# Kernel tuning notes

Hardware: AMD Instinct MI355X
Metric: run time of the kernel (lower is better)

## Reference

```python
import jax, jax.numpy as jnp
import numpy as np

EPS = 1.0 / 137.0  # fine-structure-constant epsilon used throughout the Yat ops


def yat_dense(x, W, b, alpha):
    # x: [..., C], W: [C, F] -> [..., F]
    dot = jnp.einsum('btc,cf->btf', x, W)
    x_norm = jnp.sum(x * x, axis=-1, keepdims=True)        # [..., 1]
    w_norm = jnp.sum(W * W, axis=0)                         # [F]
    dist = x_norm + w_norm - 2.0 * dot
    y = dot * dot / (dist + EPS)
    y = y + b
    F = W.shape[1]
    scale = (np.sqrt(F) / np.log(1.0 + F)) ** 1.0           # base; alpha exponent applied below
    return y * ((np.float32(np.sqrt(F)) / np.float32(np.log1p(F))) ** alpha)


def setup_inputs() -> dict:
    key = jax.random.key(0)
    ks = jax.random.split(key, 8)
    B, T, C = 4, 1024, 768
    x = jax.random.normal(ks[0], (B, T, C), dtype=jnp.float32)
    mask = jnp.tril(jnp.ones((T, T), dtype=bool))[None, None, :, :]  # causal [1,1,T,T]
    sd = 1.0 / np.sqrt(C)
    W_attn = jax.random.normal(ks[1], (C, 3 * C), dtype=jnp.float32) * sd
    b_attn = jnp.zeros((3 * C,), dtype=jnp.float32)
    alpha_attn = jnp.ones((), dtype=jnp.float32)
    W_proj = jax.random.normal(ks[2], (C, C), dtype=jnp.float32) * sd
    b_proj = jnp.zeros((C,), dtype=jnp.float32)
    alpha_proj = jnp.ones((), dtype=jnp.float32)
    return {"x": x, "mask": mask, "W_attn": W_attn, "b_attn": b_attn,
            "alpha_attn": alpha_attn, "W_proj": W_proj, "b_proj": b_proj,
            "alpha_proj": alpha_proj}


def reference(x, mask, W_attn, b_attn, alpha_attn, W_proj, b_proj, alpha_proj):
    B, T, C = x.shape
    H = 12
    D = C // H  # head_dim
    qkv = yat_dense(x, W_attn, b_attn, alpha_attn)          # [B,T,3C]
    qkv = qkv.reshape(B, T, 3 * H, D)
    q, k, v = jnp.array_split(qkv, 3, axis=2)
    q = jnp.transpose(q, (0, 2, 1, 3))                       # [B,H,T,D]
    k = jnp.transpose(k, (0, 2, 1, 3))
    v = jnp.transpose(v, (0, 2, 1, 3))
    scale = 1.0 / np.float32(np.sqrt(D))
    dot = jnp.einsum('bhid,bhjd->bhij', q, k)                # [B,H,T,T]
    sq_dot = jnp.square(dot * scale)
    q_norm = jnp.sum(jnp.square(q), axis=-1)[..., None]      # [B,H,T,1]
    k_norm = jnp.sum(jnp.square(k), axis=-1)[..., None, :]   # [B,H,1,T]
    sq_dist = q_norm + k_norm - 2.0 * dot * scale
    attn = sq_dot / (sq_dist + EPS)
    attn = jnp.where(mask, attn, jnp.finfo(jnp.float32).min)
    attn = jax.nn.softmax(attn, axis=-1)
    out = jnp.einsum('bhij,bhjd->bhid', attn, v)             # [B,H,T,D]
    out = jnp.transpose(out, (0, 2, 1, 3)).reshape(B, T, C)
    out = yat_dense(out, W_proj, b_proj, alpha_proj)         # [B,T,C]
    return out
```

## Files before the change

### kernel.cpp

```cpp
#include <hip/hip_runtime.h>
#include <math.h>

#define EPS_YAT (1.0f/137.0f)

typedef unsigned short u16;
typedef unsigned int u32;
typedef __attribute__((ext_vector_type(8))) __bf16 bf16x8;
typedef __attribute__((ext_vector_type(4))) float f32x4;

__device__ __forceinline__ float4 ld4(const float* p) { return *(const float4*)p; }

__device__ __forceinline__ u16 bf16_rne(float f) {
    u32 u = __float_as_uint(f);
    u32 r = (u + 0x7fffu + ((u >> 16) & 1u)) >> 16;
    return (u16)r;
}
__device__ __forceinline__ float bf16_f(u16 h) {
    return __uint_as_float(((u32)h) << 16);
}

__global__ void colnorm_part(const float* __restrict__ W, float* __restrict__ part,
                             int K, int N) {
    __shared__ float sm[256];
    const int col = blockIdx.x * 64 + (threadIdx.x & 63);
    const int q = threadIdx.x >> 6;
    const int rows = K >> 6;
    const int k0 = blockIdx.y * (K >> 4) + q * rows;
    float s = 0.f;
    for (int k = k0; k < k0 + rows; ++k) {
        float w = W[(size_t)k * N + col];
        s += w * w;
    }
    sm[threadIdx.x] = s;
    __syncthreads();
    if (threadIdx.x < 64)
        part[(size_t)blockIdx.y * N + col] =
            sm[threadIdx.x] + sm[threadIdx.x + 64] + sm[threadIdx.x + 128] + sm[threadIdx.x + 192];
}

__global__ void colnorm_reduce(const float* __restrict__ part, float* __restrict__ wn,
                               int N) {
    int gid = blockIdx.x * 256 + threadIdx.x;
    if (gid >= N) return;
    float s = 0.f;
    #pragma unroll
    for (int i = 0; i < 16; ++i) s += part[(size_t)i * N + gid];
    wn[gid] = s;
}

__global__ void rownorm_kernel(const float* __restrict__ X, float* __restrict__ rn, int K) {
    int wave = threadIdx.x >> 6;
    int lane = threadIdx.x & 63;
    int row = blockIdx.x * 4 + wave;
    const float* xr = X + (size_t)row * K;
    float s = 0.f;
    for (int k = lane * 4; k < K; k += 256) {
        float4 v = ld4(xr + k);
        s += v.x * v.x + v.y * v.y + v.z * v.z + v.w * v.w;
    }
    for (int off = 32; off; off >>= 1) s += __shfl_down(s, off);
    if (lane == 0) rn[row] = s;
}

__global__ void rownorm_hl(const u16* __restrict__ Xh, const u16* __restrict__ Xl,
                           float* __restrict__ rn) {
    int wave = threadIdx.x >> 6;
    int lane = threadIdx.x & 63;
    int row = blockIdx.x * 4 + wave;
    const u16* xh = Xh + (size_t)row * 768;
    const u16* xl = Xl + (size_t)row * 768;
    float s = 0.f;
    for (int k = lane * 4; k < 768; k += 256) {
        uint2 hv = *(const uint2*)(xh + k);
        uint2 lv = *(const uint2*)(xl + k);
        float a0 = bf16_f((u16)hv.x)         + bf16_f((u16)lv.x);
        float a1 = bf16_f((u16)(hv.x >> 16)) + bf16_f((u16)(lv.x >> 16));
        float a2 = bf16_f((u16)hv.y)         + bf16_f((u16)lv.y);
        float a3 = bf16_f((u16)(hv.y >> 16)) + bf16_f((u16)(lv.y >> 16));
        s += a0 * a0 + a1 * a1 + a2 * a2 + a3 * a3;
    }
    for (int off = 32; off; off >>= 1) s += __shfl_down(s, off);
    if (lane == 0) rn[row] = s;
}

__global__ void qknorm_kernel(const u16* __restrict__ qh, const u16* __restrict__ ql,
                              float* __restrict__ qn, float* __restrict__ kn) {
    int gid = blockIdx.x * 256 + threadIdx.x;
    int lane = gid & 15;
    int idx = gid >> 4;
    int which = (idx >= 49152) ? 1 : 0;
    int r = idx - which * 49152;
    int t = r & 1023;
    int bh = r >> 10;
    int h = bh % 12, b = bh / 12;
    const size_t off = (size_t)(b * 1024 + t) * 2304 + which * 768 + h * 64 + lane * 4;
    uint2 hv = *(const uint2*)(qh + off);
    uint2 lv = *(const uint2*)(ql + off);
    float a0 = bf16_f((u16)hv.x)         + bf16_f((u16)lv.x);
    float a1 = bf16_f((u16)(hv.x >> 16)) + bf16_f((u16)(lv.x >> 16));
    float a2 = bf16_f((u16)hv.y)         + bf16_f((u16)lv.y);
    float a3 = bf16_f((u16)(hv.y >> 16)) + bf16_f((u16)(lv.y >> 16));
    float s = a0 * a0 + a1 * a1 + a2 * a2 + a3 * a3;
    s += __shfl_xor(s, 1, 16);
    s += __shfl_xor(s, 2, 16);
    s += __shfl_xor(s, 4, 16);
    s += __shfl_xor(s, 8, 16);
    if (lane == 0) (which ? kn : qn)[r] = s;
}

__global__ void split_kernel(const float* __restrict__ X, u16* __restrict__ Xh,
                             u16* __restrict__ Xl, int n4) {
    int gid = blockIdx.x * 256 + threadIdx.x;
    if (gid >= n4) return;
    float4 v = ld4(X + (size_t)gid * 4);
    u16 h0 = bf16_rne(v.x), h1 = bf16_rne(v.y), h2 = bf16_rne(v.z), h3 = bf16_rne(v.w);
    u16 l0 = bf16_rne(v.x - bf16_f(h0));
    u16 l1 = bf16_rne(v.y - bf16_f(h1));
    u16 l2 = bf16_rne(v.z - bf16_f(h2));
    u16 l3 = bf16_rne(v.w - bf16_f(h3));
    uint2 hp, lp;
    hp.x = (u32)h0 | ((u32)h1 << 16); hp.y = (u32)h2 | ((u32)h3 << 16);
    lp.x = (u32)l0 | ((u32)l1 << 16); lp.y = (u32)l2 | ((u32)l3 << 16);
    *(uint2*)(Xh + (size_t)gid * 4) = hp;
    *(uint2*)(Xl + (size_t)gid * 4) = lp;
}

__global__ void split_wt_kernel(const float* __restrict__ W, u16* __restrict__ Th,
                                u16* __restrict__ Tl, int K, int N) {
    __shared__ float tile[64 * 68];
    const int tid = threadIdx.x;
    const int n0 = blockIdx.x << 6;
    const int k0 = blockIdx.y << 6;
    const int rr = tid >> 4;
    const int cc = (tid & 15) << 2;
    #pragma unroll
    for (int s = 0; s < 4; ++s) {
        int k_l = rr + s * 16;
        *(float4*)&tile[k_l * 68 + cc] = ld4(W + (size_t)(k0 + k_l) * N + n0 + cc);
    }
    __syncthreads();
    #pragma unroll
    for (int s = 0; s < 4; ++s) {
        int n_l = rr + s * 16;
        float a0 = tile[(cc + 0) * 68 + n_l];
        float a1 = tile[(cc + 1) * 68 + n_l];
        float a2 = tile[(cc + 2) * 68 + n_l];
        float a3 = tile[(cc + 3) * 68 + n_l];
        u16 h0 = bf16_rne(a0), h1 = bf16_rne(a1), h2 = bf16_rne(a2), h3 = bf16_rne(a3);
        u16 l0 = bf16_rne(a0 - bf16_f(h0));
        u16 l1 = bf16_rne(a1 - bf16_f(h1));
        u16 l2 = bf16_rne(a2 - bf16_f(h2));
        u16 l3 = bf16_rne(a3 - bf16_f(h3));
        uint2 hp, lp;
        hp.x = (u32)h0 | ((u32)h1 << 16); hp.y = (u32)h2 | ((u32)h3 << 16);
        lp.x = (u32)l0 | ((u32)l1 << 16); lp.y = (u32)l2 | ((u32)l3 << 16);
        size_t o = (size_t)(n0 + n_l) * K + k0 + cc;
        *(uint2*)(Th + o) = hp;
        *(uint2*)(Tl + o) = lp;
    }
}

template<int SPLIT>
__global__ __launch_bounds__(256, 2)
void yat_gemm_mfma(const u16* __restrict__ Ah, const u16* __restrict__ Al,
                   const u16* __restrict__ Bh, const u16* __restrict__ Bl,
                   const float* __restrict__ bias, const float* __restrict__ xn,
                   const float* __restrict__ wnc, const float* __restrict__ alphap,
                   const float Fdim, float* __restrict__ out,
                   u16* __restrict__ outh, u16* __restrict__ outl,
                   const int N, const int K) {
    __shared__ __align__(16) u16 lAh[128 * 40], lAl[128 * 40];
    __shared__ __align__(16) u16 lBh[128 * 40], lBl[128 * 40];
    const int tid = threadIdx.x;
    const int m0 = blockIdx.y << 7;
    const int n0 = blockIdx.x << 7;
    const int wave = tid >> 6;
    const int lane = tid & 63;
    const int wm = (wave >> 1) << 6;
    const int wnn = (wave & 1) << 6;
    const int lm = lane & 15;
    const int kq = lane >> 4;
    const int sr = tid >> 1;
    const int sh = (tid & 1) << 4;

    const u16* gAh = Ah + (size_t)(m0 + sr) * K + sh;
    const u16* gAl = Al + (size_t)(m0 + sr) * K + sh;
    const u16* gBh = Bh + (size_t)(n0 + sr) * K + sh;
    const u16* gBl = Bl + (size_t)(n0 + sr) * K + sh;

    f32x4 acc[4][4] = {};

    uint4 pA0 = *(const uint4*)(gAh), pA1 = *(const uint4*)(gAh + 8);
    uint4 pB0 = *(const uint4*)(gAl), pB1 = *(const uint4*)(gAl + 8);
    uint4 pC0 = *(const uint4*)(gBh), pC1 = *(const uint4*)(gBh + 8);
    uint4 pD0 = *(const uint4*)(gBl), pD1 = *(const uint4*)(gBl + 8);

    const int lw = sr * 40 + sh;
    for (int k0 = 0; k0 < K; k0 += 32) {
        __syncthreads();
        *(uint4*)&lAh[lw] = pA0; *(uint4*)&lAh[lw + 8] = pA1;
        *(uint4*)&lAl[lw] = pB0; *(uint4*)&lAl[lw + 8] = pB1;
        *(uint4*)&lBh[lw] = pC0; *(uint4*)&lBh[lw + 8] = pC1;
        *(uint4*)&lBl[lw] = pD0; *(uint4*)&lBl[lw + 8] = pD1;
        __syncthreads();
        if (k0 + 32 < K) {
            pA0 = *(const uint4*)(gAh + k0 + 32); pA1 = *(const uint4*)(gAh + k0 + 40);
            pB0 = *(const uint4*)(gAl + k0 + 32); pB1 = *(const uint4*)(gAl + k0 + 40);
            pC0 = *(const uint4*)(gBh + k0 + 32); pC1 = *(const uint4*)(gBh + k0 + 40);
            pD0 = *(const uint4*)(gBl + k0 + 32); pD1 = *(const uint4*)(gBl + k0 + 40);
        }

        bf16x8 fah[4], fal[4], fbh[4], fbl[4];
        #pragma unroll
        for (int i = 0; i < 4; ++i) {
            const int ra = (wm + i * 16 + lm) * 40 + kq * 8;
            fah[i] = *(const bf16x8*)&lAh[ra];
            fal[i] = *(const bf16x8*)&lAl[ra];
            const int rb = (wnn + i * 16 + lm) * 40 + kq * 8;
            fbh[i] = *(const bf16x8*)&lBh[rb];
            fbl[i] = *(const bf16x8*)&lBl[rb];
        }
        #pragma unroll
        for (int i = 0; i < 4; ++i)
            #pragma unroll
            for (int j = 0; j < 4; ++j) {
                f32x4 c = acc[i][j];
                c = __builtin_amdgcn_mfma_f32_16x16x32_bf16(fah[i], fbh[j], c, 0, 0, 0);
                c = __builtin_amdgcn_mfma_f32_16x16x32_bf16(fah[i], fbl[j], c, 0, 0, 0);
                c = __builtin_amdgcn_mfma_f32_16x16x32_bf16(fal[i], fbh[j], c, 0, 0, 0);
                acc[i][j] = c;
            }
    }

    const float scale = powf(sqrtf(Fdim) / log1pf(Fdim), *alphap);
    #pragma unroll
    for (int i = 0; i < 4; ++i) {
        const int mbase = m0 + wm + i * 16 + kq * 4;
        #pragma unroll
        for (int j = 0; j < 4; ++j) {
            const int n = n0 + wnn + j * 16 + lm;
            const float w2 = wnc[n];
            const float bv = bias[n];
            #pragma unroll
            for (int r = 0; r < 4; ++r) {
                const int m = mbase + r;
                float d = acc[i][j][r];
                float den = xn[m] + w2 - 2.f * d + EPS_YAT;
                float v = (d * d / den + bv) * scale;
                if constexpr (SPLIT) {
                    u16 hh = bf16_rne(v);
                    outh[(size_t)m * N + n] = hh;
                    outl[(size_t)m * N + n] = bf16_rne(v - bf16_f(hh));
                } else {
                    out[(size_t)m * N + n] = v;
                }
            }
        }
    }
}

#define MFMA_B16(a, b, c) __builtin_amdgcn_mfma_f32_16x16x32_bf16(a, b, c, 0, 0, 0)

#define ST_TILE(j) { \
    const int kro = ((j)*16 + lm) * 72 + (kq << 3); \
    bf16x8 kh = *(const bf16x8*)&KPh[kro]; \
    bf16x8 kl = *(const bf16x8*)&KPl[kro]; \
    st##j = MFMA_B16(kh, qh0, st##j); \
    st##j = MFMA_B16(kl, qh0, st##j); \
    st##j = MFMA_B16(kh, ql0, st##j); \
    kh = *(const bf16x8*)&KPh[kro + 32]; \
    kl = *(const bf16x8*)&KPl[kro + 32]; \
    st##j = MFMA_B16(kh, qh1, st##j); \
    st##j = MFMA_B16(kl, qh1, st##j); \
    st##j = MFMA_B16(kh, ql1, st##j); \
}

#define YAT_EL(j, r) { \
    float sv = st##j[r] * 0.125f; \
    float den = qnm + kns[(j)*16 + kq4 + (r)] - 2.f * sv + EPS_YAT; \
    float v = sv * sv / den; \
    if (diag && ((j)*16 + kq4 + (r) > wband + lm)) v = -3e38f; \
    st##j[r] = v; mm = fmaxf(mm, v); }
#define YAT_TILE(j) YAT_EL(j,0) YAT_EL(j,1) YAT_EL(j,2) YAT_EL(j,3)

#define PEXP_TILE(j) { \
    float p0 = __expf(st##j[0] - mnew), p1 = __expf(st##j[1] - mnew); \
    float p2 = __expf(st##j[2] - mnew), p3 = __expf(st##j[3] - mnew); \
    rs += p0 + p1 + p2 + p3; \
    u16 h0 = bf16_rne(p0), h1 = bf16_rne(p1), h2 = bf16_rne(p2), h3 = bf16_rne(p3); \
    uint2 hp; hp.x = (u32)h0 | ((u32)h1 << 16); hp.y = (u32)h2 | ((u32)h3 << 16); \
    *(uint2*)&KPh[pmrow + (j)*16 + kq4] = hp; \
    u16 e0 = bf16_rne(p0 - bf16_f(h0)), e1 = bf16_rne(p1 - bf16_f(h1)); \
    u16 e2 = bf16_rne(p2 - bf16_f(h2)), e3 = bf16_rne(p3 - bf16_f(h3)); \
    uint2 lp; lp.x = (u32)e0 | ((u32)e1 << 16); lp.y = (u32)e2 | ((u32)e3 << 16); \
    *(uint2*)&KPl[pmrow + (j)*16 + kq4] = lp; }

#define PV_TILE(j) { \
    const int vro = ((j)*16 + lm) * 72 + vkq8; \
    bf16x8 vh = *(const bf16x8*)&Vth[vro]; \
    bf16x8 vl = *(const bf16x8*)&Vtl[vro]; \
    ac##j = MFMA_B16(ph0, vh, ac##j); \
    ac##j = MFMA_B16(pl0, vh, ac##j); \
    ac##j = MFMA_B16(ph0, vl, ac##j); \
    vh = *(const bf16x8*)&Vth[vro + 32]; \
    vl = *(const bf16x8*)&Vtl[vro + 32]; \
    ac##j = MFMA_B16(ph1, vh, ac##j); \
    ac##j = MFMA_B16(pl1, vh, ac##j); \
    ac##j = MFMA_B16(ph1, vl, ac##j); \
}

#define WRVT(dst, v2, m) { \
    dst[(sj * 4 + 16 * (m) + 0) * 72 + toks] = (u16)((v2).x); \
    dst[(sj * 4 + 16 * (m) + 1) * 72 + toks] = (u16)((v2).x >> 16); \
    dst[(sj * 4 + 16 * (m) + 2) * 72 + toks] = (u16)((v2).y); \
    dst[(sj * 4 + 16 * (m) + 3) * 72 + toks] = (u16)((v2).y >> 16); }

__global__ __launch_bounds__(256, 4)
void yat_flash_mfma(const u16* __restrict__ qh_g, const u16* __restrict__ ql_g,
                    const float* __restrict__ qn, const float* __restrict__ kn,
                    u16* __restrict__ outh, u16* __restrict__ outl) {
    __shared__ __align__(16) u16 KPh[64 * 72], KPl[64 * 72];
    __shared__ __align__(16) u16 Vth[64 * 72], Vtl[64 * 72];
    __shared__ float kns[64];

    const int tid = threadIdx.x;
    const int L = blockIdx.x;
    const int u = L / 48;
    const int qt = (u & 1) ? (u >> 1) : (15 - (u >> 1));
    const int bh = L % 48;
    const int h = bh % 12, b = bh / 12;
    const int wave = tid >> 6;
    const int lane = tid & 63;
    const int lm = lane & 15;
    const int kq = lane >> 4;
    const int kq4 = kq << 2;
    const int wband = wave << 4;
    const int sr = tid >> 2;
    const int sj = tid & 3;
    const int toks = sr ^ (sj << 3);
    const int vkq8 = (kq ^ (lm >> 2)) << 3;
    const size_t base = (size_t)(b * 1024) * 2304 + h * 64;

    {
        const size_t qoff = base + (size_t)((qt << 6) + sr) * 2304 + sj * 16;
        *(uint4*)&KPh[sr * 72 + sj * 16]     = *(const uint4*)(qh_g + qoff);
        *(uint4*)&KPh[sr * 72 + sj * 16 + 8] = *(const uint4*)(qh_g + qoff + 8);
        *(uint4*)&KPl[sr * 72 + sj * 16]     = *(const uint4*)(ql_g + qoff);
        *(uint4*)&KPl[sr * 72 + sj * 16 + 8] = *(const uint4*)(ql_g + qoff + 8);
    }
    const float qnm = qn[bh * 1024 + (qt << 6) + wband + lm];

    const size_t r0 = base + (size_t)sr * 2304;
    uint4 kh0 = *(const uint4*)(qh_g + r0 + 768 + sj * 16);
    uint4 kh1 = *(const uint4*)(qh_g + r0 + 768 + sj * 16 + 8);
    uint4 kl0 = *(const uint4*)(ql_g + r0 + 768 + sj * 16);
    uint4 kl1 = *(const uint4*)(ql_g + r0 + 768 + sj * 16 + 8);
    uint2 vh0 = *(const uint2*)(qh_g + r0 + 1536 + sj * 4);
    uint2 vh1 = *(const uint2*)(qh_g + r0 + 1536 + sj * 4 + 16);
    uint2 vh2 = *(const uint2*)(qh_g + r0 + 1536 + sj * 4 + 32);
    uint2 vh3 = *(const uint2*)(qh_g + r0 + 1536 + sj * 4 + 48);
    uint2 vl0 = *(const uint2*)(ql_g + r0 + 1536 + sj * 4);
    uint2 vl1 = *(const uint2*)(ql_g + r0 + 1536 + sj * 4 + 16);
    uint2 vl2 = *(const uint2*)(ql_g + r0 + 1536 + sj * 4 + 32);
    uint2 vl3 = *(const uint2*)(ql_g + r0 + 1536 + sj * 4 + 48);
    float knS = (tid < 64) ? kn[bh * 1024 + tid] : 0.f;

    __syncthreads();

    const int qrow = (wband + lm) * 72;
    const bf16x8 qh0 = *(const bf16x8*)&KPh[qrow + (kq << 3)];
    const bf16x8 qh1 = *(const bf16x8*)&KPh[qrow + 32 + (kq << 3)];
    const bf16x8 ql0 = *(const bf16x8*)&KPl[qrow + (kq << 3)];
    const bf16x8 ql1 = *(const bf16x8*)&KPl[qrow + 32 + (kq << 3)];

    f32x4 ac0 = {}, ac1 = {}, ac2 = {}, ac3 = {};
    float mrun = -3e38f, lrun = 0.f;
    const int pmrow = (wband + lm) * 72;

    for (int kt = 0; kt <= qt; ++kt) {
        __syncthreads();
        *(uint4*)&KPh[sr * 72 + sj * 16]     = kh0;
        *(uint4*)&KPh[sr * 72 + sj * 16 + 8] = kh1;
        *(uint4*)&KPl[sr * 72 + sj * 16]     = kl0;
        *(uint4*)&KPl[sr * 72 + sj * 16 + 8] = kl1;
        WRVT(Vth, vh0, 0) WRVT(Vth, vh1, 1) WRVT(Vth, vh2, 2) WRVT(Vth, vh3, 3)
        WRVT(Vtl, vl0, 0) WRVT(Vtl, vl1, 1) WRVT(Vtl, vl2, 2) WRVT(Vtl, vl3, 3)
        if (tid < 64) kns[tid] = knS;
        __syncthreads();

        if (kt < qt) {
            const size_t r = base + (size_t)(((kt + 1) << 6) + sr) * 2304;
            kh0 = *(const uint4*)(qh_g + r + 768 + sj * 16);
            kh1 = *(const uint4*)(qh_g + r + 768 + sj * 16 + 8);
            kl0 = *(const uint4*)(ql_g + r + 768 + sj * 16);
            kl1 = *(const uint4*)(ql_g + r + 768 + sj * 16 + 8);
            vh0 = *(const uint2*)(qh_g + r + 1536 + sj * 4);
            vh1 = *(const uint2*)(qh_g + r + 1536 + sj * 4 + 16);
            vh2 = *(const uint2*)(qh_g + r + 1536 + sj * 4 + 32);
            vh3 = *(const uint2*)(qh_g + r + 1536 + sj * 4 + 48);
            vl0 = *(const uint2*)(ql_g + r + 1536 + sj * 4);
            vl1 = *(const uint2*)(ql_g + r + 1536 + sj * 4 + 16);
            vl2 = *(const uint2*)(ql_g + r + 1536 + sj * 4 + 32);
            vl3 = *(const uint2*)(ql_g + r + 1536 + sj * 4 + 48);
            if (tid < 64) knS = kn[bh * 1024 + ((kt + 1) << 6) + tid];
        }

        f32x4 st0 = {}, st1 = {}, st2 = {}, st3 = {};
        __builtin_amdgcn_s_setprio(1);
        ST_TILE(0) ST_TILE(1) ST_TILE(2) ST_TILE(3)
        __builtin_amdgcn_s_setprio(0);
        __syncthreads();

        const bool diag = (kt == qt);
        float mm = -3e38f;
        YAT_TILE(0) YAT_TILE(1) YAT_TILE(2) YAT_TILE(3)
        mm = fmaxf(mm, __shfl_xor(mm, 16));
        mm = fmaxf(mm, __shfl_xor(mm, 32));
        const float mnew = fmaxf(mrun, mm);
        const float al = __expf(mrun - mnew);
        mrun = mnew;
        float rs = 0.f;
        PEXP_TILE(0) PEXP_TILE(1) PEXP_TILE(2) PEXP_TILE(3)
        rs += __shfl_xor(rs, 16);
        rs += __shfl_xor(rs, 32);
        lrun = lrun * al + rs;
        const float a0 = __shfl(al, kq4 + 0, 16);
        const float a1 = __shfl(al, kq4 + 1, 16);
        const float a2 = __shfl(al, kq4 + 2, 16);
        const float a3 = __shfl(al, kq4 + 3, 16);
        ac0[0] *= a0; ac0[1] *= a1; ac0[2] *= a2; ac0[3] *= a3;
        ac1[0] *= a0; ac1[1] *= a1; ac1[2] *= a2; ac1[3] *= a3;
        ac2[0] *= a0; ac2[1] *= a1; ac2[2] *= a2; ac2[3] *= a3;
        ac3[0] *= a0; ac3[1] *= a1; ac3[2] *= a2; ac3[3] *= a3;
        __syncthreads();

        const bf16x8 ph0 = *(const bf16x8*)&KPh[pmrow + (kq << 3)];
        const bf16x8 ph1 = *(const bf16x8*)&KPh[pmrow + 32 + (kq << 3)];
        const bf16x8 pl0 = *(const bf16x8*)&KPl[pmrow + (kq << 3)];
        const bf16x8 pl1 = *(const bf16x8*)&KPl[pmrow + 32 + (kq << 3)];
        __builtin_amdgcn_s_setprio(1);
        PV_TILE(0) PV_TILE(1) PV_TILE(2) PV_TILE(3)
        __builtin_amdgcn_s_setprio(0);
    }

    const float i0 = 1.f / __shfl(lrun, kq4 + 0, 16);
    const float i1 = 1.f / __shfl(lrun, kq4 + 1, 16);
    const float i2 = 1.f / __shfl(lrun, kq4 + 2, 16);
    const float i3 = 1.f / __shfl(lrun, kq4 + 3, 16);
    const size_t obase = (size_t)(b * 1024 + (qt << 6) + wband + kq4) * 768 + h * 64 + lm;
    u16* oph = outh + obase;
    u16* opl = outl + obase;
    #define STORE_E(j, r, iv) { \
        float ov = ac##j[r] * iv; \
        u16 hh = bf16_rne(ov); \
        oph[(size_t)(r) * 768 + (j)*16] = hh; \
        opl[(size_t)(r) * 768 + (j)*16] = bf16_rne(ov - bf16_f(hh)); }
    #define STORE_T(j) { STORE_E(j,0,i0) STORE_E(j,1,i1) STORE_E(j,2,i2) STORE_E(j,3,i3) }
    STORE_T(0) STORE_T(1) STORE_T(2) STORE_T(3)
    #undef STORE_T
    #undef STORE_E
}

extern "C" void kernel_launch(void* const* d_in, const int* in_sizes, int n_in,
                              void* d_out, int out_size, void* d_ws, size_t ws_size,
                              hipStream_t stream) {
    const float* x          = (const float*)d_in[0];
    const float* W_attn     = (const float*)d_in[2];
    const float* b_attn     = (const float*)d_in[3];
    const float* alpha_attn = (const float*)d_in[4];
    const float* W_proj     = (const float*)d_in[5];
    const float* b_proj     = (const float*)d_in[6];
    const float* alpha_proj = (const float*)d_in[7];

    float* ws       = (float*)d_ws;
    u16*   qkvh     = (u16*)ws;
    u16*   qkvl     = (u16*)(ws + 4718592);
    float* xn       = ws + 12582912;
    float* an       = ws + 12587008;
    float* wn_attn  = ws + 12591104;
    float* wn_proj  = ws + 12593408;
    float* qn       = ws + 12594176;
    float* kn       = ws + 12643328;

    float* cn_part_a = ws + 9437184;
    float* cn_part_p = ws + 9437184 + 36864;
    u16* xh  = (u16*)(ws + 9437184);
    u16* xl  = (u16*)(ws + 11010048);
    u16* aoh = (u16*)(ws + 9437184);
    u16* aol = (u16*)(ws + 11010048);
    u16* wth = (u16*)d_out;
    u16* wtl = (u16*)d_out + 1769472;
    u16* wph = (u16*)(ws + 3145728);
    u16* wpl = (u16*)(ws + 3440640);

    colnorm_part<<<dim3(36, 16), 256, 0, stream>>>(W_attn, cn_part_a, 768, 2304);
    colnorm_part<<<dim3(12, 16), 256, 0, stream>>>(W_proj, cn_part_p, 768, 768);
    colnorm_reduce<<<9, 256, 0, stream>>>(cn_part_a, wn_attn, 2304);
    colnorm_reduce<<<3, 256, 0, stream>>>(cn_part_p, wn_proj, 768);
    rownorm_kernel<<<1024, 256, 0, stream>>>(x, xn, 768);
    split_kernel<<<3072, 256, 0, stream>>>(x, xh, xl, 786432);
    split_wt_kernel<<<dim3(36, 12), 256, 0, stream>>>(W_attn, wth, wtl, 768, 2304);
    yat_gemm_mfma<1><<<dim3(18, 32), 256, 0, stream>>>(
        xh, xl, wth, wtl, b_attn, xn, wn_attn, alpha_attn, 2304.f,
        nullptr, qkvh, qkvl, 2304, 768);
    qknorm_kernel<<<6144, 256, 0, stream>>>(qkvh, qkvl, qn, kn);
    yat_flash_mfma<<<768, 256, 0, stream>>>(qkvh, qkvl, qn, kn, aoh, aol);
    rownorm_hl<<<1024, 256, 0, stream>>>(aoh, aol, an);
    split_wt_kernel<<<dim3(12, 12), 256, 0, stream>>>(W_proj, wph, wpl, 768, 768);
    yat_gemm_mfma<0><<<dim3(6, 32), 256, 0, stream>>>(
        aoh, aol, wph, wpl, b_proj, an, wn_proj, alpha_proj, 768.f,
        (float*)d_out, nullptr, nullptr, 768, 768);
}
```

Before: 278.5 us.

## Use direct global-to-LDS loads with double buffering in split-bf16 GEMM

Replaces register-staged global loads plus LDS stores with global_load_lds direct-to-LDS transfers into a double-buffered shared tile, so the next K-slice streams in while MFMAs run on the current one. This removes one barrier per iteration and the VGPRs that held the prefetched data. The LDS row stride drops from 40 to 32 halfwords with no padding, which risks bank conflicts on the fragment reads. Doubling the LDS buffers may also limit occupancy.

```diff
diff --git a/kernel.cpp b/kernel.cpp
--- a/kernel.cpp
+++ b/kernel.cpp
@@ -17,6 +17,13 @@
 }
 __device__ __forceinline__ float bf16_f(u16 h) {
     return __uint_as_float(((u32)h) << 16);
+}
+
+__device__ __forceinline__ void glds16(const u16* g, u16* s) {
+    __builtin_amdgcn_global_load_lds(
+        (const __attribute__((address_space(1))) void*)g,
+        (__attribute__((address_space(3))) void*)s,
+        16, 0, 0);
 }
 
 __global__ void colnorm_part(const float* __restrict__ W, float* __restrict__ part,
@@ -169,54 +176,59 @@
                    const float Fdim, float* __restrict__ out,
                    u16* __restrict__ outh, u16* __restrict__ outl,
                    const int N, const int K) {
-    __shared__ __align__(16) u16 lAh[128 * 40], lAl[128 * 40];
-    __shared__ __align__(16) u16 lBh[128 * 40], lBl[128 * 40];
+    __shared__ __align__(16) u16 lds[2 * 4 * 4096];
     const int tid = threadIdx.x;
     const int m0 = blockIdx.y << 7;
     const int n0 = blockIdx.x << 7;
-    const int wave = tid >> 6;
-    const int lane = tid & 63;
-    const int wm = (wave >> 1) << 6;
-    const int wnn = (wave & 1) << 6;
-    const int lm = lane & 15;
-    const int kq = lane >> 4;
-    const int sr = tid >> 1;
-    const int sh = (tid & 1) << 4;
-
-    const u16* gAh = Ah + (size_t)(m0 + sr) * K + sh;
-    const u16* gAl = Al + (size_t)(m0 + sr) * K + sh;
-    const u16* gBh = Bh + (size_t)(n0 + sr) * K + sh;
-    const u16* gBl = Bl + (size_t)(n0 + sr) * K + sh;
+    const int w = tid >> 6;
+    const int l = tid & 63;
+    const int wm = (w >> 1) << 6;
+    const int wnn = (w & 1) << 6;
+    const int lm = l & 15;
+    const int kq = l >> 4;
+
+    const int srow = 16 * w + (l >> 2);
+    const int scol = (l & 3) << 3;
+    const u16* gA1 = Ah + (size_t)(m0 + srow) * K + scol;
+    const u16* gA2 = Ah + (size_t)(m0 + 64 + srow) * K + scol;
+    const u16* gC1 = Al + (size_t)(m0 + srow) * K + scol;
+    const u16* gC2 = Al + (size_t)(m0 + 64 + srow) * K + scol;
+    const u16* gB1 = Bh + (size_t)(n0 + srow) * K + scol;
+    const u16* gB2 = Bh + (size_t)(n0 + 64 + srow) * K + scol;
+    const u16* gD1 = Bl + (size_t)(n0 + srow) * K + scol;
+    const u16* gD2 = Bl + (size_t)(n0 + 64 + srow) * K + scol;
+    const int wb = w * 512;
 
     f32x4 acc[4][4] = {};
 
-    uint4 pA0 = *(const uint4*)(gAh), pA1 = *(const uint4*)(gAh + 8);
-    uint4 pB0 = *(const uint4*)(gAl), pB1 = *(const uint4*)(gAl + 8);
-    uint4 pC0 = *(const uint4*)(gBh), pC1 = *(const uint4*)(gBh + 8);
-    uint4 pD0 = *(const uint4*)(gBl), pD1 = *(const uint4*)(gBl + 8);
-
-    const int lw = sr * 40 + sh;
+    #define STAGE(buf, kk) { \
+        u16* sb = lds + (buf) * 16384; \
+        glds16(gA1 + (kk), sb + wb); \
+        glds16(gA2 + (kk), sb + 2048 + wb); \
+        glds16(gC1 + (kk), sb + 4096 + wb); \
+        glds16(gC2 + (kk), sb + 6144 + wb); \
+        glds16(gB1 + (kk), sb + 8192 + wb); \
+        glds16(gB2 + (kk), sb + 10240 + wb); \
+        glds16(gD1 + (kk), sb + 12288 + wb); \
+        glds16(gD2 + (kk), sb + 14336 + wb); }
+
+    STAGE(0, 0);
+    __syncthreads();
+    int cur = 0;
     for (int k0 = 0; k0 < K; k0 += 32) {
-        __syncthreads();
-        *(uint4*)&lAh[lw] = pA0; *(uint4*)&lAh[lw + 8] = pA1;
-        *(uint4*)&lAl[lw] = pB0; *(uint4*)&lAl[lw + 8] = pB1;
-        *(uint4*)&lBh[lw] = pC0; *(uint4*)&lBh[lw + 8] = pC1;
-        *(uint4*)&lBl[lw] = pD0; *(uint4*)&lBl[lw + 8] = pD1;
-        __syncthreads();
-        if (k0 + 32 < K) {
-            pA0 = *(const uint4*)(gAh + k0 + 32); pA1 = *(const uint4*)(gAh + k0 + 40);
-            pB0 = *(const uint4*)(gAl + k0 + 32); pB1 = *(const uint4*)(gAl + k0 + 40);
-            pC0 = *(const uint4*)(gBh + k0 + 32); pC1 = *(const uint4*)(gBh + k0 + 40);
-            pD0 = *(const uint4*)(gBl + k0 + 32); pD1 = *(const uint4*)(gBl + k0 + 40);
-        }
+        if (k0 + 32 < K) STAGE(cur ^ 1, k0 + 32);
+        const u16* lAh = lds + cur * 16384;
+        const u16* lAl = lAh + 4096;
+        const u16* lBh = lAh + 8192;
+        const u16* lBl = lAh + 12288;
 
         bf16x8 fah[4], fal[4], fbh[4], fbl[4];
         #pragma unroll
         for (int i = 0; i < 4; ++i) {
-            const int ra = (wm + i * 16 + lm) * 40 + kq * 8;
+            const int ra = (wm + i * 16 + lm) * 32 + kq * 8;
             fah[i] = *(const bf16x8*)&lAh[ra];
             fal[i] = *(const bf16x8*)&lAl[ra];
-            const int rb = (wnn + i * 16 + lm) * 40 + kq * 8;
+            const int rb = (wnn + i * 16 + lm) * 32 + kq * 8;
             fbh[i] = *(const bf16x8*)&lBh[rb];
             fbl[i] = *(const bf16x8*)&lBl[rb];
         }
@@ -230,7 +242,10 @@
                 c = __builtin_amdgcn_mfma_f32_16x16x32_bf16(fal[i], fbh[j], c, 0, 0, 0);
                 acc[i][j] = c;
             }
-    }
+        __syncthreads();
+        cur ^= 1;
+    }
+    #undef STAGE
 
     const float scale = powf(sqrtf(Fdim) / log1pf(Fdim), *alphap);
     #pragma unroll
```

New measurement: 276.0 us. About the same (-0.9%).
